# Performance work log

Measured on AMD Instinct MI355X. Metric: run time of the kernel, lower is better.

The kernel has to match this reference:

```python
import jax, jax.numpy as jnp
import numpy as np
import math

E = 1024
H = 16
D = E // H  # head_dim = 64


def setup_inputs() -> dict:
    key = jax.random.key(0)
    ks = jax.random.split(key, 12)
    B, N = 2, 2048
    x = jax.random.normal(ks[0], (B, N, E), dtype=jnp.float32)
    region_mask = jax.random.randint(ks[1], (B, N), 0, 2).astype(jnp.float32)
    attn_mask = jax.random.randint(ks[2], (B, N, N), 0, 2).astype(bool)
    std = 0.02
    Wq = jax.random.normal(ks[3], (E, E), dtype=jnp.float32) * std
    Wk = jax.random.normal(ks[4], (E, E), dtype=jnp.float32) * std
    Wv = jax.random.normal(ks[5], (E, E), dtype=jnp.float32) * std
    Wo = jax.random.normal(ks[6], (E, E), dtype=jnp.float32) * std
    bq = jnp.zeros((E,), jnp.float32)
    bk = jnp.zeros((E,), jnp.float32)
    bv = jnp.zeros((E,), jnp.float32)
    bo = jnp.zeros((E,), jnp.float32)
    region_bias = jax.random.normal(ks[7], (1, H, 1, 1), dtype=jnp.float32) * std
    return {"x": x, "region_mask": region_mask, "attn_mask": attn_mask,
            "Wq": Wq, "bq": bq, "Wk": Wk, "bk": bk, "Wv": Wv, "bv": bv,
            "Wo": Wo, "bo": bo, "region_bias": region_bias}


def reference(x, region_mask, attn_mask, Wq, bq, Wk, bk, Wv, bv, Wo, bo, region_bias):
    B, N, _ = x.shape
    # projections (torch Linear: y = x @ W.T + b), split heads -> (B, H, N, D)
    def split_heads(y):
        return y.reshape(B, N, H, D).transpose(0, 2, 1, 3)
    q = split_heads(x @ Wq.T + bq)
    k = split_heads(x @ Wk.T + bk)
    v = split_heads(x @ Wv.T + bv)
    # eager scores (B, H, N, N)
    scores = jnp.einsum('bhqd,bhkd->bhqk', q, k) / math.sqrt(D)
    # additive regional bias: (1,H,1,1) * (B,1,N,1) broadcasts over keys
    scores = scores + region_bias * region_mask[:, None, :, None]
    # masked_fill(attn_mask, -inf); mask is (B,N,N) -> (B,1,N,N)
    scores = jnp.where(attn_mask[:, None, :, :], -jnp.inf, scores)
    w = jax.nn.softmax(scores, axis=-1)  # dropout is identity in eval
    out = jnp.einsum('bhqk,bhkd->bhqd', w, v)
    out = out.transpose(0, 2, 1, 3).reshape(B, N, E)
    return out @ Wo.T + bo
```

## Files before the change

### kernel.cpp

```cpp
#include <hip/hip_runtime.h>
#include <hip/hip_bf16.h>
#include <stdint.h>

typedef __hip_bfloat16 bf16;
typedef unsigned long long u64;
typedef __attribute__((ext_vector_type(4))) float f32x4;
typedef __attribute__((ext_vector_type(8))) short short8;

#define MFMA16 __builtin_amdgcn_mfma_f32_16x16x32_bf16

constexpr int Bc = 2, Nc = 2048, Ec = 1024, Hc = 16, Dc = 64;
constexpr int Mc = Bc * Nc;
constexpr int Kc = Ec;

constexpr size_t OFF_XB   = 256;
constexpr size_t SZ_XE    = (size_t)Mc * Ec * 2;
constexpr size_t SZ_W     = (size_t)Ec * Ec * 2;
constexpr size_t OFF_WQB  = OFF_XB  + SZ_XE;
constexpr size_t OFF_WKB  = OFF_WQB + SZ_W;
constexpr size_t OFF_WVB  = OFF_WKB + SZ_W;
constexpr size_t OFF_WOB  = OFF_WVB + SZ_W;
constexpr size_t OFF_QB   = OFF_WOB + SZ_W;
constexpr size_t OFF_KB   = OFF_QB  + SZ_XE;
constexpr size_t OFF_VTB  = OFF_KB  + SZ_XE;
constexpr size_t OFF_OB   = OFF_VTB + SZ_XE;
constexpr size_t OFF_MP   = OFF_OB  + SZ_XE;

#define QSCALE 0.18033688f

__device__ __forceinline__ void gld16(const void* g, void* l) {
  __builtin_amdgcn_global_load_lds((const __attribute__((address_space(1))) void*)g,
                                   (__attribute__((address_space(3))) void*)l,
                                   16, 0, 0);
}

__device__ __forceinline__ float fexp2(float x) {
#if __has_builtin(__builtin_amdgcn_exp2f)
  return __builtin_amdgcn_exp2f(x);
#else
  float r; asm("v_exp_f32 %0, %1" : "=v"(r) : "v"(x)); return r;
#endif
}

__device__ __forceinline__ unsigned cvt2(float a, float b) {
  __hip_bfloat162 h = __float22bfloat162_rn(float2{a, b});
  return *reinterpret_cast<unsigned*>(&h);
}

__device__ __forceinline__ unsigned nib4(unsigned x) {
  const unsigned b = ((x & 0x7F7F7F7Fu) + 0x7F7F7F7Fu) | x;
  return ((b >> 7) & 1u) | ((b >> 14) & 2u) | ((b >> 21) & 4u) | ((b >> 28) & 8u);
}

__global__ __launch_bounds__(256)
void prep(const unsigned char* __restrict__ mbytes,
          const float* __restrict__ x,  const float* __restrict__ wq,
          const float* __restrict__ wk, const float* __restrict__ wv,
          const float* __restrict__ wo,
          u64* __restrict__ packed,
          uint2* __restrict__ xb,  uint2* __restrict__ wqb,
          uint2* __restrict__ wkb, uint2* __restrict__ wvb,
          uint2* __restrict__ wob)
{
  if (blockIdx.x < 512) {
    __shared__ int found;
    if (threadIdx.x == 0) found = 0;
    __syncthreads();
    int loc = 0;
    for (int i = threadIdx.x; i < 4096; i += 256)
      if ((i & 3) && mbytes[i] == 1) loc = 1;
    if (loc) atomicOr(&found, 1);
    __syncthreads();
    const bool bytem = (found != 0);

    const int widx = blockIdx.x * 256 + threadIdx.x;
    u64 bits = 0;
    if (bytem) {
      const uint4* src = (const uint4*)(mbytes + (size_t)widx * 64);
#pragma unroll
      for (int i = 0; i < 4; ++i) {
        const uint4 v = src[i];
        bits |= (u64)nib4(v.x) << (16 * i + 0);
        bits |= (u64)nib4(v.y) << (16 * i + 4);
        bits |= (u64)nib4(v.z) << (16 * i + 8);
        bits |= (u64)nib4(v.w) << (16 * i + 12);
      }
    } else {
      const uint4* src = (const uint4*)mbytes + (size_t)widx * 16;
#pragma unroll
      for (int i = 0; i < 16; ++i) {
        const uint4 v = src[i];
        const unsigned n = (v.x != 0 ? 1u : 0u) | (v.y != 0 ? 2u : 0u) |
                           (v.z != 0 ? 4u : 0u) | (v.w != 0 ? 8u : 0u);
        bits |= (u64)n << (4 * i);
      }
    }
    packed[widx] = bits;
    return;
  }
  const long XG = (long)Mc * Ec / 4;
  const long WG = (long)Ec * Ec / 4;
  const long total = XG + 4 * WG;
  const long nthr = (long)(gridDim.x - 512) * 256;
  for (long g = (long)(blockIdx.x - 512) * 256 + threadIdx.x; g < total; g += nthr) {
    const float* src; uint2* dst; long r;
    if (g < XG)              { src = x;  dst = xb;  r = g; }
    else if (g < XG + WG)    { src = wq; dst = wqb; r = g - XG; }
    else if (g < XG + 2*WG)  { src = wk; dst = wkb; r = g - XG - WG; }
    else if (g < XG + 3*WG)  { src = wv; dst = wvb; r = g - XG - 2*WG; }
    else                     { src = wo; dst = wob; r = g - XG - 3*WG; }
    float4 v = reinterpret_cast<const float4*>(src)[r];
    uint2 o;
    o.x = cvt2(v.x, v.y);
    o.y = cvt2(v.z, v.w);
    dst[r] = o;
  }
}

__device__ __forceinline__ void gemm_core(const bf16* __restrict__ A,
                                          const bf16* __restrict__ Bw,
                                          int bm, int bn,
                                          bf16* As0, bf16* As1,
                                          bf16* Bs0, bf16* Bs1,
                                          f32x4 (&acc)[4][4])
{
  const int t = threadIdx.x, lane = t & 63, w = t >> 6;
  const int wr = w >> 1, wc = w & 1;
  const int llo = lane & 15, lhi = lane >> 4;
  const int srow = t >> 3, schunk = t & 7;
  const int sswz = schunk ^ (srow & 7);
  const bf16* aSrc = A  + (size_t)(bm * 128 + srow) * Kc + sswz * 8;
  const bf16* bSrc = Bw + (size_t)(bn * 128 + srow) * Kc + sswz * 8;

  auto stage = [&](bf16* Asb, bf16* Bsb, int kt) {
    char* ldsA = (char*)Asb + w * 1024;
    char* ldsB = (char*)Bsb + w * 1024;
#pragma unroll
    for (int i = 0; i < 4; ++i) {
      gld16(aSrc + (size_t)i * 32 * Kc + kt, ldsA + i * 4096);
      gld16(bSrc + (size_t)i * 32 * Kc + kt, ldsB + i * 4096);
    }
  };

  stage(As0, Bs0, 0);
  __syncthreads();

  for (int kti = 0; kti < Kc / 64; ++kti) {
    const bool even = !(kti & 1);
    const char* Asc = (const char*)(even ? As0 : As1);
    const char* Bsc = (const char*)(even ? Bs0 : Bs1);
    if (kti + 1 < Kc / 64)
      stage(even ? As1 : As0, even ? Bs1 : Bs0, (kti + 1) * 64);
#pragma unroll
    for (int kk = 0; kk < 2; ++kk) {
      short8 af[4], bg[4];
#pragma unroll
      for (int i = 0; i < 4; ++i) {
        const int chunk = (kk * 4 + lhi) ^ (lane & 7);
        const int rowa = wr * 64 + i * 16 + llo;
        const int rowb = wc * 64 + i * 16 + llo;
        af[i] = *(const short8*)(Asc + rowa * 128 + chunk * 16);
        bg[i] = *(const short8*)(Bsc + rowb * 128 + chunk * 16);
      }
#pragma unroll
      for (int i = 0; i < 4; ++i)
#pragma unroll
        for (int j = 0; j < 4; ++j)
          acc[i][j] = MFMA16(af[i], bg[j], acc[i][j], 0, 0, 0);
    }
    __syncthreads();
  }
}

__global__ __launch_bounds__(256)
void gemm_qkv(const bf16* __restrict__ xb,
              const bf16* __restrict__ wq, const bf16* __restrict__ wk,
              const bf16* __restrict__ wv,
              const float* __restrict__ bq, const float* __restrict__ bk,
              const float* __restrict__ bv,
              bf16* __restrict__ Q, bf16* __restrict__ Ko, bf16* __restrict__ VT)
{
  __shared__ bf16 As[2][128 * 64], Bs[2][128 * 64];
  const int sel = blockIdx.x >> 8, inner = blockIdx.x & 255;
  const int bm = inner >> 3, bn = inner & 7;
  const bf16*  W    = sel == 0 ? wq : (sel == 1 ? wk : wv);
  const float* bias = sel == 0 ? bq : (sel == 1 ? bk : bv);
  f32x4 acc[4][4] = {};
  gemm_core(xb, W, bm, bn, As[0], As[1], Bs[0], Bs[1], acc);

  const int t = threadIdx.x, lane = t & 63, w = t >> 6;
  const int wr = w >> 1, wc = w & 1;
  const int llo = lane & 15, lhi = lane >> 4;
#pragma unroll
  for (int i = 0; i < 4; ++i)
#pragma unroll
    for (int j = 0; j < 4; ++j)
#pragma unroll
      for (int r = 0; r < 4; ++r) {
        const int m = bm * 128 + wr * 64 + i * 16 + lhi * 4 + r;
        const int e = bn * 128 + wc * 64 + j * 16 + llo;
        float v = acc[i][j][r] + bias[e];
        if (sel == 0) {
          Q[(size_t)m * Ec + e] = __float2bfloat16(v * QSCALE);
        } else if (sel == 1) {
          Ko[(size_t)m * Ec + e] = __float2bfloat16(v);
        } else {
          const int b = m >> 11, n = m & 2047, h = e >> 6, d = e & 63;
          VT[(((size_t)(b * Hc + h)) * Dc + d) * Nc + n] = __float2bfloat16(v);
        }
      }
}

__global__ __launch_bounds__(256)
void gemm_out(const bf16* __restrict__ ob, const bf16* __restrict__ wo,
              const float* __restrict__ bo, float* __restrict__ out)
{
  __shared__ bf16 As[2][128 * 64], Bs[2][128 * 64];
  const int bm = blockIdx.x >> 3, bn = blockIdx.x & 7;
  f32x4 acc[4][4] = {};
  gemm_core(ob, wo, bm, bn, As[0], As[1], Bs[0], Bs[1], acc);

  const int t = threadIdx.x, lane = t & 63, w = t >> 6;
  const int wr = w >> 1, wc = w & 1;
  const int llo = lane & 15, lhi = lane >> 4;
#pragma unroll
  for (int i = 0; i < 4; ++i)
#pragma unroll
    for (int j = 0; j < 4; ++j)
#pragma unroll
      for (int r = 0; r < 4; ++r) {
        const int m = bm * 128 + wr * 64 + i * 16 + lhi * 4 + r;
        const int e = bn * 128 + wc * 64 + j * 16 + llo;
        out[(size_t)m * Ec + e] = acc[i][j][r] + bo[e];
      }
}

__global__ __launch_bounds__(512, 6)
void flash_attn(const bf16* __restrict__ Q, const bf16* __restrict__ Kb,
                const bf16* __restrict__ VT, const u64* __restrict__ mpack,
                bf16* __restrict__ O)
{
  __shared__ bf16 Ks[2][64 * 64];
  __shared__ bf16 Vs[2][64 * 64];
  __shared__ bf16 Ps[8][16 * 64];
  const int t = threadIdx.x, lane = t & 63, w = t >> 6;
  const int bh = blockIdx.x >> 4, qt = blockIdx.x & 15;
  const int b = bh >> 4, h = bh & 15;
  const int q0 = qt * 128 + w * 16;
  const int llo = lane & 15, lhi = lane >> 4;
  const int swz = (lane & 7) << 4;

  short8 aq0, aq1;
  {
    const bf16* qb = Q + ((size_t)(b * Nc + q0 + llo)) * Ec + h * Dc + lhi * 8;
    aq0 = *(const short8*)qb;
    aq1 = *(const short8*)(qb + 32);
  }

  const short8 kOnes = {16256,16256,16256,16256,16256,16256,16256,16256};
  const f32x4 fz = {};
  f32x4 oacc[4] = {};
  f32x4 lacc = {};

  const int srow = t >> 3, schunk = t & 7;
  const int sswz = schunk ^ (srow & 7);
  const bf16* kSrc = Kb + ((size_t)(b * Nc + srow)) * Ec + h * Dc + sswz * 8;
  const bf16* vSrc = VT + ((size_t)(bh * Dc + srow)) * Nc + sswz * 8;

  const u64* mrow = mpack + ((size_t)(b * Nc) + q0 + llo) * (Nc / 64);

  auto stage = [&](int buf, int kt) {
    gld16(kSrc + (size_t)kt * Ec, (char*)Ks[buf] + w * 1024);
    gld16(vSrc + kt,              (char*)Vs[buf] + w * 1024);
  };

  stage(0, 0);
  __syncthreads();

  char* prow = (char*)Ps[w] + llo * 128;

  for (int ti = 0; ti < Nc / 64; ++ti) {
    const int cur = ti & 1;
    if (ti + 1 < Nc / 64) stage(cur ^ 1, (ti + 1) * 64);
    u64 mw = mrow[ti];

    const char* KsC = (const char*)Ks[cur];
    const char* VsC = (const char*)Vs[cur];

    f32x4 s[4];
    __builtin_amdgcn_s_setprio(1);
#pragma unroll
    for (int f = 0; f < 4; ++f) {
      const int row = f * 16 + llo;
      short8 kb0 = *(const short8*)(KsC + row * 128 + (((0 + lhi) * 16) ^ swz));
      short8 kb1 = *(const short8*)(KsC + row * 128 + (((4 + lhi) * 16) ^ swz));
      s[f] = MFMA16(kb0, aq0, fz, 0, 0, 0);
      s[f] = MFMA16(kb1, aq1, s[f], 0, 0, 0);
    }
    __builtin_amdgcn_s_setprio(0);

    const unsigned mlo = (unsigned)(mw >> (lhi * 4));
    const unsigned mhi = (unsigned)(mw >> (lhi * 4 + 32));
#pragma unroll
    for (int f = 0; f < 4; ++f) {
      const unsigned mf = (f < 2 ? (mlo >> (f * 16)) : (mhi >> ((f - 2) * 16)));
#pragma unroll
      for (int r = 0; r < 4; ++r) {
        const float p = fexp2(s[f][r]);
        s[f][r] = ((mf >> r) & 1u) ? 0.f : p;
      }
    }

#pragma unroll
    for (int f = 0; f < 4; ++f) {
      uint2 pk;
      pk.x = cvt2(s[f][0], s[f][1]);
      pk.y = cvt2(s[f][2], s[f][3]);
      *(uint2*)(prow + ((f * 32 + lhi * 8) ^ swz)) = pk;
    }
    asm volatile("s_waitcnt lgkmcnt(0)" ::: "memory");

    short8 pa0 = *(const short8*)(prow + ((0 * 64 + lhi * 16) ^ swz));
    short8 pa1 = *(const short8*)(prow + ((1 * 64 + lhi * 16) ^ swz));

    __builtin_amdgcn_s_setprio(1);
#pragma unroll
    for (int df = 0; df < 4; ++df) {
      const int row = df * 16 + llo;
      short8 vb0 = *(const short8*)(VsC + row * 128 + (((0 + lhi) * 16) ^ swz));
      short8 vb1 = *(const short8*)(VsC + row * 128 + (((4 + lhi) * 16) ^ swz));
      oacc[df] = MFMA16(pa0, vb0, oacc[df], 0, 0, 0);
      oacc[df] = MFMA16(pa1, vb1, oacc[df], 0, 0, 0);
    }
    lacc = MFMA16(pa0, kOnes, lacc, 0, 0, 0);
    lacc = MFMA16(pa1, kOnes, lacc, 0, 0, 0);
    __builtin_amdgcn_s_setprio(0);
    __syncthreads();
  }

  float inv[4];
#pragma unroll
  for (int r = 0; r < 4; ++r) inv[r] = 1.0f / lacc[r];
#pragma unroll
  for (int df = 0; df < 4; ++df)
#pragma unroll
    for (int r = 0; r < 4; ++r) {
      const int q = q0 + lhi * 4 + r;
      const int e = h * Dc + df * 16 + llo;
      O[((size_t)(b * Nc + q)) * Ec + e] = __float2bfloat16(oacc[df][r] * inv[r]);
    }
}

extern "C" void kernel_launch(void* const* d_in, const int* in_sizes, int n_in,
                              void* d_out, int out_size, void* d_ws, size_t ws_size,
                              hipStream_t stream)
{
  (void)in_sizes; (void)n_in; (void)out_size; (void)ws_size;
  const float* x  = (const float*)d_in[0];
  const void* mask = d_in[2];
  const float* Wq = (const float*)d_in[3];
  const float* bq = (const float*)d_in[4];
  const float* Wk = (const float*)d_in[5];
  const float* bk = (const float*)d_in[6];
  const float* Wv = (const float*)d_in[7];
  const float* bv = (const float*)d_in[8];
  const float* Wo = (const float*)d_in[9];
  const float* bo = (const float*)d_in[10];
  float* out = (float*)d_out;
  char* ws = (char*)d_ws;

  bf16* XB  = (bf16*)(ws + OFF_XB);
  bf16* WQB = (bf16*)(ws + OFF_WQB);
  bf16* WKB = (bf16*)(ws + OFF_WKB);
  bf16* WVB = (bf16*)(ws + OFF_WVB);
  bf16* WOB = (bf16*)(ws + OFF_WOB);
  bf16* QB  = (bf16*)(ws + OFF_QB);
  bf16* KB  = (bf16*)(ws + OFF_KB);
  bf16* VTB = (bf16*)(ws + OFF_VTB);
  bf16* OB  = (bf16*)(ws + OFF_OB);
  u64*  MP  = (u64*)(ws + OFF_MP);

  prep<<<512 + 1280, 256, 0, stream>>>((const unsigned char*)mask,
                                       x, Wq, Wk, Wv, Wo, MP,
                                       (uint2*)XB, (uint2*)WQB, (uint2*)WKB,
                                       (uint2*)WVB, (uint2*)WOB);
  gemm_qkv<<<768, 256, 0, stream>>>(XB, WQB, WKB, WVB, bq, bk, bv, QB, KB, VTB);
  flash_attn<<<512, 512, 0, stream>>>(QB, KB, VTB, MP, OB);
  gemm_out<<<256, 256, 0, stream>>>(OB, WOB, bo, out);
}
```

Before: 138.9 us.

## Halve GEMM N-tile to 64, unroll attention loop by two, relax occupancy

The GEMM core is templated on the N tile width, and both the QKV and output projections now use 128x64 tiles, doubling the block count so the GPU's compute units are better filled. The flash-attention loop is manually unrolled by two with fixed LDS buffer indices, and the mask word for the next tile is prefetched. Its launch bound drops from 6 to 4 waves-per-EU so the compiler has more registers to work with. Smaller GEMM tiles reduce per-block data reuse and add more global loads per FLOP.

```diff
diff --git a/kernel.cpp b/kernel.cpp
--- a/kernel.cpp
+++ b/kernel.cpp
@@ -117,29 +117,32 @@
   }
 }
 
+template<int BN>
 __device__ __forceinline__ void gemm_core(const bf16* __restrict__ A,
                                           const bf16* __restrict__ Bw,
                                           int bm, int bn,
                                           bf16* As0, bf16* As1,
                                           bf16* Bs0, bf16* Bs1,
-                                          f32x4 (&acc)[4][4])
-{
+                                          f32x4 (&acc)[4][BN / 32])
+{
+  constexpr int NJ = BN / 32;
   const int t = threadIdx.x, lane = t & 63, w = t >> 6;
   const int wr = w >> 1, wc = w & 1;
   const int llo = lane & 15, lhi = lane >> 4;
   const int srow = t >> 3, schunk = t & 7;
   const int sswz = schunk ^ (srow & 7);
   const bf16* aSrc = A  + (size_t)(bm * 128 + srow) * Kc + sswz * 8;
-  const bf16* bSrc = Bw + (size_t)(bn * 128 + srow) * Kc + sswz * 8;
+  const bf16* bSrc = Bw + (size_t)(bn * BN  + srow) * Kc + sswz * 8;
 
   auto stage = [&](bf16* Asb, bf16* Bsb, int kt) {
     char* ldsA = (char*)Asb + w * 1024;
     char* ldsB = (char*)Bsb + w * 1024;
 #pragma unroll
-    for (int i = 0; i < 4; ++i) {
+    for (int i = 0; i < 4; ++i)
       gld16(aSrc + (size_t)i * 32 * Kc + kt, ldsA + i * 4096);
+#pragma unroll
+    for (int i = 0; i < BN / 32; ++i)
       gld16(bSrc + (size_t)i * 32 * Kc + kt, ldsB + i * 4096);
-    }
   };
 
   stage(As0, Bs0, 0);
@@ -153,19 +156,22 @@
       stage(even ? As1 : As0, even ? Bs1 : Bs0, (kti + 1) * 64);
 #pragma unroll
     for (int kk = 0; kk < 2; ++kk) {
-      short8 af[4], bg[4];
+      short8 af[4], bg[NJ];
+      const int chunk = (kk * 4 + lhi) ^ (lane & 7);
 #pragma unroll
       for (int i = 0; i < 4; ++i) {
-        const int chunk = (kk * 4 + lhi) ^ (lane & 7);
         const int rowa = wr * 64 + i * 16 + llo;
-        const int rowb = wc * 64 + i * 16 + llo;
         af[i] = *(const short8*)(Asc + rowa * 128 + chunk * 16);
-        bg[i] = *(const short8*)(Bsc + rowb * 128 + chunk * 16);
+      }
+#pragma unroll
+      for (int j = 0; j < NJ; ++j) {
+        const int rowb = wc * (BN / 2) + j * 16 + llo;
+        bg[j] = *(const short8*)(Bsc + rowb * 128 + chunk * 16);
       }
 #pragma unroll
       for (int i = 0; i < 4; ++i)
 #pragma unroll
-        for (int j = 0; j < 4; ++j)
+        for (int j = 0; j < NJ; ++j)
           acc[i][j] = MFMA16(af[i], bg[j], acc[i][j], 0, 0, 0);
     }
     __syncthreads();
@@ -180,13 +186,13 @@
               const float* __restrict__ bv,
               bf16* __restrict__ Q, bf16* __restrict__ Ko, bf16* __restrict__ VT)
 {
-  __shared__ bf16 As[2][128 * 64], Bs[2][128 * 64];
-  const int sel = blockIdx.x >> 8, inner = blockIdx.x & 255;
-  const int bm = inner >> 3, bn = inner & 7;
+  __shared__ bf16 As[2][128 * 64], Bs[2][64 * 64];
+  const int sel = blockIdx.x >> 9, inner = blockIdx.x & 511;
+  const int bm = inner >> 4, bn = inner & 15;
   const bf16*  W    = sel == 0 ? wq : (sel == 1 ? wk : wv);
   const float* bias = sel == 0 ? bq : (sel == 1 ? bk : bv);
-  f32x4 acc[4][4] = {};
-  gemm_core(xb, W, bm, bn, As[0], As[1], Bs[0], Bs[1], acc);
+  f32x4 acc[4][2] = {};
+  gemm_core<64>(xb, W, bm, bn, As[0], As[1], Bs[0], Bs[1], acc);
 
   const int t = threadIdx.x, lane = t & 63, w = t >> 6;
   const int wr = w >> 1, wc = w & 1;
@@ -194,11 +200,11 @@
 #pragma unroll
   for (int i = 0; i < 4; ++i)
 #pragma unroll
-    for (int j = 0; j < 4; ++j)
+    for (int j = 0; j < 2; ++j)
 #pragma unroll
       for (int r = 0; r < 4; ++r) {
         const int m = bm * 128 + wr * 64 + i * 16 + lhi * 4 + r;
-        const int e = bn * 128 + wc * 64 + j * 16 + llo;
+        const int e = bn * 64 + wc * 32 + j * 16 + llo;
         float v = acc[i][j][r] + bias[e];
         if (sel == 0) {
           Q[(size_t)m * Ec + e] = __float2bfloat16(v * QSCALE);
@@ -215,10 +221,10 @@
 void gemm_out(const bf16* __restrict__ ob, const bf16* __restrict__ wo,
               const float* __restrict__ bo, float* __restrict__ out)
 {
-  __shared__ bf16 As[2][128 * 64], Bs[2][128 * 64];
-  const int bm = blockIdx.x >> 3, bn = blockIdx.x & 7;
-  f32x4 acc[4][4] = {};
-  gemm_core(ob, wo, bm, bn, As[0], As[1], Bs[0], Bs[1], acc);
+  __shared__ bf16 As[2][128 * 64], Bs[2][64 * 64];
+  const int bm = blockIdx.x >> 4, bn = blockIdx.x & 15;
+  f32x4 acc[4][2] = {};
+  gemm_core<64>(ob, wo, bm, bn, As[0], As[1], Bs[0], Bs[1], acc);
 
   const int t = threadIdx.x, lane = t & 63, w = t >> 6;
   const int wr = w >> 1, wc = w & 1;
@@ -226,16 +232,16 @@
 #pragma unroll
   for (int i = 0; i < 4; ++i)
 #pragma unroll
-    for (int j = 0; j < 4; ++j)
+    for (int j = 0; j < 2; ++j)
 #pragma unroll
       for (int r = 0; r < 4; ++r) {
         const int m = bm * 128 + wr * 64 + i * 16 + lhi * 4 + r;
-        const int e = bn * 128 + wc * 64 + j * 16 + llo;
+        const int e = bn * 64 + wc * 32 + j * 16 + llo;
         out[(size_t)m * Ec + e] = acc[i][j][r] + bo[e];
       }
 }
 
-__global__ __launch_bounds__(512, 6)
+__global__ __launch_bounds__(512, 4)
 void flash_attn(const bf16* __restrict__ Q, const bf16* __restrict__ Kb,
                 const bf16* __restrict__ VT, const u64* __restrict__ mpack,
                 bf16* __restrict__ O)
@@ -274,19 +280,9 @@
     gld16(vSrc + kt,              (char*)Vs[buf] + w * 1024);
   };
 
-  stage(0, 0);
-  __syncthreads();
-
   char* prow = (char*)Ps[w] + llo * 128;
 
-  for (int ti = 0; ti < Nc / 64; ++ti) {
-    const int cur = ti & 1;
-    if (ti + 1 < Nc / 64) stage(cur ^ 1, (ti + 1) * 64);
-    u64 mw = mrow[ti];
-
-    const char* KsC = (const char*)Ks[cur];
-    const char* VsC = (const char*)Vs[cur];
-
+  auto body = [&](const char* KsC, const char* VsC, u64 mw) {
     f32x4 s[4];
     __builtin_amdgcn_s_setprio(1);
 #pragma unroll
@@ -335,7 +331,22 @@
     lacc = MFMA16(pa0, kOnes, lacc, 0, 0, 0);
     lacc = MFMA16(pa1, kOnes, lacc, 0, 0, 0);
     __builtin_amdgcn_s_setprio(0);
+  };
+
+  stage(0, 0);
+  __syncthreads();
+  u64 mw = mrow[0];
+
+  for (int ti = 0; ti < Nc / 64; ti += 2) {
+    if (ti + 1 < Nc / 64) stage(1, (ti + 1) * 64);
+    const u64 mwB = (ti + 1 < Nc / 64) ? mrow[ti + 1] : 0;
+    body((const char*)Ks[0], (const char*)Vs[0], mw);
     __syncthreads();
+    if (ti + 2 < Nc / 64) stage(0, (ti + 2) * 64);
+    const u64 mwA = (ti + 2 < Nc / 64) ? mrow[ti + 2] : 0;
+    body((const char*)Ks[1], (const char*)Vs[1], mwB);
+    __syncthreads();
+    mw = mwA;
   }
 
   float inv[4];
@@ -384,7 +395,7 @@
                                        x, Wq, Wk, Wv, Wo, MP,
                                        (uint2*)XB, (uint2*)WQB, (uint2*)WKB,
                                        (uint2*)WVB, (uint2*)WOB);
-  gemm_qkv<<<768, 256, 0, stream>>>(XB, WQB, WKB, WVB, bq, bk, bv, QB, KB, VTB);
+  gemm_qkv<<<1536, 256, 0, stream>>>(XB, WQB, WKB, WVB, bq, bk, bv, QB, KB, VTB);
   flash_attn<<<512, 512, 0, stream>>>(QB, KB, VTB, MP, OB);
-  gemm_out<<<256, 256, 0, stream>>>(OB, WOB, bo, out);
-}
+  gemm_out<<<512, 256, 0, stream>>>(OB, WOB, bo, out);
+}
```

Measured after the change: 139.6 us. About the same (+0.5%).
